# Kernel optimization log

Hardware: AMD Instinct MI355X
Metric: run time of the kernel (lower is better)

## Reference

```python
import jax, jax.numpy as jnp
import numpy as np

K_SELECT = 100      # select_box_nums_for_evaluation
IOU_THR = 0.7       # nms_iou_threshold
CONF_THR = 0.3      # confidence_score


def setup_inputs() -> dict:
    key = jax.random.key(0)
    k1, k2, k3 = jax.random.split(key, 3)
    B, Q, C = 256, 900, 91
    pred_logits = jax.random.normal(k1, (B, Q, C), dtype=jnp.float32)
    # cxcywh boxes in (0,1), strictly positive w/h
    pred_boxes = jax.random.uniform(k2, (B, Q, 4), dtype=jnp.float32, minval=0.05, maxval=0.45)
    # (img_h, img_w) per image
    target_sizes = jax.random.uniform(k3, (B, 2), dtype=jnp.float32, minval=200.0, maxval=1000.0)
    return {"pred_logits": pred_logits, "pred_boxes": pred_boxes, "target_sizes": target_sizes}


def _pairwise_iou(boxes):
    # boxes: [K,4] xyxy -> iou [K,K]
    area = (boxes[:, 2] - boxes[:, 0]) * (boxes[:, 3] - boxes[:, 1])
    lt = jnp.maximum(boxes[:, None, :2], boxes[None, :, :2])
    rb = jnp.minimum(boxes[:, None, 2:], boxes[None, :, 2:])
    wh = jnp.clip(rb - lt, 0.0)
    inter = wh[..., 0] * wh[..., 1]
    union = area[:, None] + area[None, :] - inter
    return inter / jnp.maximum(union, 1e-9)


def _nms_mask(boxes):
    # boxes already sorted by descending score (top_k output order).
    # Greedy NMS: box i suppresses lower-scored j if iou > IOU_THR and i itself kept.
    K = boxes.shape[0]
    iou = _pairwise_iou(boxes)
    rng = jnp.arange(K)

    def body(i, keep):
        suppress = (iou[i] > IOU_THR) & keep[i] & (rng > i)
        return keep & ~suppress

    return jax.lax.fori_loop(0, K, body, jnp.ones((K,), dtype=bool))


def reference(pred_logits, pred_boxes, target_sizes):
    B, Q, C = pred_logits.shape
    prob = jax.nn.sigmoid(pred_logits).reshape(B, Q * C)
    scores, topk_idx = jax.lax.top_k(prob, K_SELECT)        # [B,K] sorted desc
    topk_boxes = topk_idx // C                               # query index
    labels = topk_idx % C                                    # class index

    # cxcywh -> xyxy
    cxcy, wh = pred_boxes[..., :2], pred_boxes[..., 2:]
    xyxy = jnp.concatenate([cxcy - 0.5 * wh, cxcy + 0.5 * wh], axis=-1)  # [B,Q,4]
    boxes = jnp.take_along_axis(xyxy, topk_boxes[..., None], axis=1)     # [B,K,4]

    img_h, img_w = target_sizes[:, 0], target_sizes[:, 1]
    scale_fct = jnp.stack([img_w, img_h, img_w, img_h], axis=1)          # [B,4]
    boxes = boxes * scale_fct[:, None, :]

    conf_keep = scores > CONF_THR                            # confidence filter
    nms_keep = jax.vmap(_nms_mask)(boxes)                    # per-image NMS
    keep = conf_keep & nms_keep                              # fixed-shape mask (ragged lists in torch)
    return scores, labels, boxes, keep
```

## Files before the change

kernel.cpp:

```cpp
#include <hip/hip_runtime.h>
#include <stdint.h>

#define NBATCH 256
#define NQ 900
#define NC 91
#define NQC (NQ * NC)
#define KSEL 100
#define IOU_THRF 0.7f
#define CONF_THRF 0.3f
#define TH_LOGIT 2.2f
#define DELTA 4096u

#define SLC 8
#define SF4FULL 2560
#define SF4LAST 2555
#define ANT 256
#define SCAP 256
#define CAPB (SLC * SCAP)

#define BNT 512
#define HBINS 64
#define SRTCAP 512

__device__ __forceinline__ uint32_t fkey(float x) {
  uint32_t b = __float_as_uint(x);
  return b ^ ((uint32_t)((int32_t)b >> 31) | 0x80000000u);
}
__device__ __forceinline__ float unfkey(uint32_t k) {
  uint32_t b = (k & 0x80000000u) ? (k ^ 0x80000000u) : ~k;
  return __uint_as_float(b);
}
__device__ __forceinline__ float sigmoidf_ref(float x) {
  return 1.0f / (1.0f + expf(-x));
}

__global__ __launch_bounds__(ANT) void kfilter(const float* __restrict__ logits,
                                               uint32_t* __restrict__ cnts,
                                               unsigned long long* __restrict__ cand) {
  __shared__ unsigned long long lbuf[SCAP];
  __shared__ uint32_t lcnt;

  const int blk = blockIdx.x;
  const int b = blk / SLC;
  const int s = blk - b * SLC;
  const int tid = threadIdx.x;
  const int sf4 = (s == SLC - 1) ? SF4LAST : SF4FULL;
  const float4* lg4 = (const float4*)(logits + (size_t)b * NQC) + (size_t)s * SF4FULL;

  if (tid == 0) lcnt = 0;
  __syncthreads();

  for (int i = tid; i < sf4; i += ANT) {
    float4 v = lg4[i];
    const uint32_t ibase = (uint32_t)((s * SF4FULL + i) * 4);
    if (v.x >= TH_LOGIT) {
      uint32_t p = atomicAdd(&lcnt, 1u);
      if (p < SCAP) lbuf[p] = (((unsigned long long)fkey(v.x)) << 32) | (ibase + 0);
    }
    if (v.y >= TH_LOGIT) {
      uint32_t p = atomicAdd(&lcnt, 1u);
      if (p < SCAP) lbuf[p] = (((unsigned long long)fkey(v.y)) << 32) | (ibase + 1);
    }
    if (v.z >= TH_LOGIT) {
      uint32_t p = atomicAdd(&lcnt, 1u);
      if (p < SCAP) lbuf[p] = (((unsigned long long)fkey(v.z)) << 32) | (ibase + 2);
    }
    if (v.w >= TH_LOGIT) {
      uint32_t p = atomicAdd(&lcnt, 1u);
      if (p < SCAP) lbuf[p] = (((unsigned long long)fkey(v.w)) << 32) | (ibase + 3);
    }
  }
  __syncthreads();
  const uint32_t m = lcnt;
  if (tid == 0) cnts[blk] = m;
  const uint32_t mw = m < SCAP ? m : SCAP;
  for (uint32_t i = tid; i < mw; i += ANT)
    cand[(size_t)blk * SCAP + i] = lbuf[i];
}

union BSMem {
  struct {
    unsigned long long keys[CAPB];
    unsigned long long srt[SRTCAP];
    unsigned long long ranked[KSEL];
  } p;
  struct {
    float iou[KSEL * KSEL];
    float box[KSEL][4];
    int keep[KSEL];
  } nms;
};

__global__ __launch_bounds__(BNT) void merge_nms(const uint32_t* __restrict__ cnts,
                                                 const unsigned long long* __restrict__ cand,
                                                 const float* __restrict__ logits,
                                                 const float* __restrict__ pboxes,
                                                 const float* __restrict__ tsizes,
                                                 float* __restrict__ out,
                                                 int force_fallback) {
  __shared__ BSMem sm;
  __shared__ unsigned long long rankbuf[KSEL];
  __shared__ uint32_t scnt[SLC], soff[SLC];
  __shared__ uint32_t s_hist[HBINS];
  __shared__ uint32_t s_n, s_bad, s_cut, s_m;
  __shared__ unsigned long long red[BNT / 64];
  __shared__ unsigned long long s_last;

  const int b = blockIdx.x;
  const int tid = threadIdx.x;
  const float* lg = logits + (size_t)b * NQC;

  bool good = !force_fallback;
  if (good) {
    if (tid < SLC) scnt[tid] = cnts[b * SLC + tid];
    __syncthreads();
    if (tid == 0) {
      uint32_t off = 0, bad = 0;
      for (int i = 0; i < SLC; i++) {
        soff[i] = off;
        if (scnt[i] > SCAP) bad = 1;
        off += scnt[i];
      }
      s_n = off;
      s_bad = bad | (off < KSEL ? 1u : 0u);
    }
    __syncthreads();
    good = (s_bad == 0);
  }
  const uint32_t n = good ? s_n : 0;

  if (good) {
    const int wid = tid >> 6, lane = tid & 63;
    for (int sl = wid; sl < SLC; sl += BNT / 64) {
      const uint32_t c = scnt[sl], o = soff[sl];
      for (uint32_t j = lane; j < c; j += 64)
        sm.p.keys[o + j] = cand[((size_t)b * SLC + sl) * SCAP + j];
    }
    if (tid < HBINS) s_hist[tid] = 0;
    if (tid == 0) s_m = 0;
    __syncthreads();

    for (uint32_t i = tid; i < n; i += BNT) {
      uint32_t k = (uint32_t)(sm.p.keys[i] >> 32);
      uint32_t bin = (k >> 20) - 0xC00u;
      if (bin > HBINS - 1) bin = HBINS - 1;
      atomicAdd(&s_hist[bin], 1u);
    }
    __syncthreads();

    if (tid < 64) {
      uint32_t h = s_hist[tid];
      uint32_t suf = h;
      #pragma unroll
      for (int off = 1; off < 64; off <<= 1) {
        uint32_t t = __shfl_down(suf, off);
        if (tid + off < 64) suf += t;
      }
      bool pred = (suf >= KSEL) && (suf - h < KSEL);
      unsigned long long mask = __ballot(pred);
      int cutlane = __ffsll((long long)mask) - 1;
      if (tid == 0) s_cut = (uint32_t)cutlane;
    }
    __syncthreads();
    const uint32_t cut = s_cut;
    if (cut >= HBINS - 1) good = false;
    const uint32_t thresh = ((cut + 0xC00u) << 20) - DELTA;

    if (good) {
      for (uint32_t i = tid; i < n; i += BNT) {
        unsigned long long key = sm.p.keys[i];
        uint32_t k = (uint32_t)(key >> 32);
        if (k >= thresh) {
          uint32_t pb = __float_as_uint(sigmoidf_ref(unfkey(k)));
          uint32_t pos = atomicAdd(&s_m, 1u);
          if (pos < SRTCAP)
            sm.p.srt[pos] = (((unsigned long long)(~pb)) << 32) |
                            (key & 0xFFFFFFFFULL);
        }
      }
      __syncthreads();
      const uint32_t m = s_m;
      if (m > SRTCAP) good = false;
      if (good) {
        for (uint32_t q = tid; q < m; q += BNT) {
          unsigned long long mykey = sm.p.srt[q];
          uint32_t r = 0;
          for (uint32_t j = 0; j < m; j++)
            r += (sm.p.srt[j] < mykey) ? 1u : 0u;
          if (r < KSEL) rankbuf[r] = mykey;
        }
        __syncthreads();
      }
    }
  }

  if (!good) {
    unsigned long long last = ~0ULL;
    for (int r = 0; r < KSEL; r++) {
      unsigned long long best = 0ULL;
      for (int i = tid; i < NQC; i += BNT) {
        uint32_t pb = __float_as_uint(sigmoidf_ref(lg[i]));
        unsigned long long cmp = (((unsigned long long)pb) << 32) |
                                 (unsigned long long)(~(uint32_t)i);
        if (cmp < last && cmp > best) best = cmp;
      }
      #pragma unroll
      for (int o = 32; o >= 1; o >>= 1) {
        unsigned long long other = __shfl_down(best, o);
        if (other > best) best = other;
      }
      if ((tid & 63) == 0) red[tid >> 6] = best;
      __syncthreads();
      if (tid == 0) {
        unsigned long long mx = red[0];
        for (int w = 1; w < BNT / 64; w++) if (red[w] > mx) mx = red[w];
        s_last = mx;
        uint32_t pb = (uint32_t)(mx >> 32);
        uint32_t id = ~(uint32_t)mx;
        rankbuf[r] = (((unsigned long long)(~pb)) << 32) | (unsigned long long)id;
      }
      __syncthreads();
      last = s_last;
    }
  }

  float score = 0.0f;
  int idx = 0;
  if (tid < KSEL) {
    unsigned long long key = rankbuf[tid];
    score = __uint_as_float(~(uint32_t)(key >> 32));
    idx = (int)(uint32_t)(key & 0xFFFFFFFFu);
  }
  __syncthreads();

  const float img_h = tsizes[b * 2 + 0];
  const float img_w = tsizes[b * 2 + 1];
  float* out_scores = out;
  float* out_labels = out + (size_t)NBATCH * KSEL;
  float* out_boxes  = out + (size_t)2 * NBATCH * KSEL;
  float* out_keep   = out + (size_t)2 * NBATCH * KSEL + (size_t)NBATCH * KSEL * 4;

  if (tid < KSEL) {
    int q = idx / NC;
    int lab = idx - q * NC;
    const float* pb = pboxes + ((size_t)b * NQ + q) * 4;
    float cx = pb[0], cy = pb[1], w = pb[2], h = pb[3];
    float hw = __fmul_rn(0.5f, w), hh = __fmul_rn(0.5f, h);
    float x0 = __fmul_rn(__fsub_rn(cx, hw), img_w);
    float y0 = __fmul_rn(__fsub_rn(cy, hh), img_h);
    float x1 = __fmul_rn(__fadd_rn(cx, hw), img_w);
    float y1 = __fmul_rn(__fadd_rn(cy, hh), img_h);
    out_scores[(size_t)b * KSEL + tid] = score;
    out_labels[(size_t)b * KSEL + tid] = (float)lab;
    float* ob = out_boxes + ((size_t)b * KSEL + tid) * 4;
    ob[0] = x0; ob[1] = y0; ob[2] = x1; ob[3] = y1;
    sm.nms.box[tid][0] = x0; sm.nms.box[tid][1] = y0;
    sm.nms.box[tid][2] = x1; sm.nms.box[tid][3] = y1;
  }
  __syncthreads();

  for (int e = tid; e < KSEL * KSEL; e += BNT) {
    int i = e / KSEL;
    int j = e - i * KSEL;
    float ax0 = sm.nms.box[i][0], ay0 = sm.nms.box[i][1];
    float ax1 = sm.nms.box[i][2], ay1 = sm.nms.box[i][3];
    float bx0 = sm.nms.box[j][0], by0 = sm.nms.box[j][1];
    float bx1 = sm.nms.box[j][2], by1 = sm.nms.box[j][3];
    float areaA = __fmul_rn(__fsub_rn(ax1, ax0), __fsub_rn(ay1, ay0));
    float areaB = __fmul_rn(__fsub_rn(bx1, bx0), __fsub_rn(by1, by0));
    float ltx = fmaxf(ax0, bx0), lty = fmaxf(ay0, by0);
    float rbx = fminf(ax1, bx1), rby = fminf(ay1, by1);
    float wx = fmaxf(__fsub_rn(rbx, ltx), 0.0f);
    float wy = fmaxf(__fsub_rn(rby, lty), 0.0f);
    float inter = __fmul_rn(wx, wy);
    float uni = __fsub_rn(__fadd_rn(areaA, areaB), inter);
    sm.nms.iou[e] = __fdiv_rn(inter, fmaxf(uni, 1e-9f));
  }
  __syncthreads();

  if (tid < 64) {
    int keepA = 1;
    int keepB = 1;
    for (int i = 0; i < KSEL; i++) {
      int owner = i & 63;
      int ki = (i < 64) ? __shfl(keepA, owner) : __shfl(keepB, owner);
      if (ki) {
        if (tid > i && sm.nms.iou[i * KSEL + tid] > IOU_THRF) keepA = 0;
        int j = tid + 64;
        if (j < KSEL && j > i && sm.nms.iou[i * KSEL + j] > IOU_THRF) keepB = 0;
      }
    }
    sm.nms.keep[tid] = keepA;
    if (tid + 64 < KSEL) sm.nms.keep[tid + 64] = keepB;
  }
  __syncthreads();

  if (tid < KSEL) {
    float kp = (score > CONF_THRF && sm.nms.keep[tid]) ? 1.0f : 0.0f;
    out_keep[(size_t)b * KSEL + tid] = kp;
  }
}

extern "C" void kernel_launch(void* const* d_in, const int* in_sizes, int n_in,
                              void* d_out, int out_size, void* d_ws, size_t ws_size,
                              hipStream_t stream) {
  const float* logits = (const float*)d_in[0];
  const float* pboxes = (const float*)d_in[1];
  const float* tsizes = (const float*)d_in[2];
  (void)in_sizes; (void)n_in; (void)out_size;

  const size_t cnt_bytes = ((size_t)NBATCH * SLC * sizeof(uint32_t) + 255) & ~(size_t)255;
  const size_t need = cnt_bytes +
                      (size_t)NBATCH * SLC * SCAP * sizeof(unsigned long long);
  if (ws_size >= need) {
    uint32_t* cnts = (uint32_t*)d_ws;
    unsigned long long* cand = (unsigned long long*)((char*)d_ws + cnt_bytes);
    kfilter<<<NBATCH * SLC, ANT, 0, stream>>>(logits, cnts, cand);
    merge_nms<<<NBATCH, BNT, 0, stream>>>(cnts, cand, logits, pboxes, tsizes,
                                          (float*)d_out, 0);
  } else {
    merge_nms<<<NBATCH, BNT, 0, stream>>>(nullptr, nullptr, logits, pboxes, tsizes,
                                          (float*)d_out, 1);
  }
}
```

Baseline: 47.54 us.

## Fuse candidate filter into single per-image postprocessing kernel

Merges the separate filtering kernel (8 slices per image, 2048 blocks) into the merge/NMS kernel, so each 1024-thread block scans its image's logits directly and appends candidates into shared memory. This removes the second launch and the global workspace round trip for candidates and counts. In exchange, only 256 blocks stream the 84 MB logits tensor, which lowers memory-level parallelism on a GPU with many CUs, and a single shared-memory atomic counter per block becomes a contention point.

```diff
diff --git a/kernel.cpp b/kernel.cpp
--- a/kernel.cpp
+++ b/kernel.cpp
@@ -5,20 +5,15 @@
 #define NQ 900
 #define NC 91
 #define NQC (NQ * NC)
+#define NV4 (NQC / 4)
 #define KSEL 100
 #define IOU_THRF 0.7f
 #define CONF_THRF 0.3f
 #define TH_LOGIT 2.2f
 #define DELTA 4096u
 
-#define SLC 8
-#define SF4FULL 2560
-#define SF4LAST 2555
-#define ANT 256
-#define SCAP 256
-#define CAPB (SLC * SCAP)
-
-#define BNT 512
+#define NT 1024
+#define CAPB 2048
 #define HBINS 64
 #define SRTCAP 512
 
@@ -34,55 +29,10 @@
   return 1.0f / (1.0f + expf(-x));
 }
 
-__global__ __launch_bounds__(ANT) void kfilter(const float* __restrict__ logits,
-                                               uint32_t* __restrict__ cnts,
-                                               unsigned long long* __restrict__ cand) {
-  __shared__ unsigned long long lbuf[SCAP];
-  __shared__ uint32_t lcnt;
-
-  const int blk = blockIdx.x;
-  const int b = blk / SLC;
-  const int s = blk - b * SLC;
-  const int tid = threadIdx.x;
-  const int sf4 = (s == SLC - 1) ? SF4LAST : SF4FULL;
-  const float4* lg4 = (const float4*)(logits + (size_t)b * NQC) + (size_t)s * SF4FULL;
-
-  if (tid == 0) lcnt = 0;
-  __syncthreads();
-
-  for (int i = tid; i < sf4; i += ANT) {
-    float4 v = lg4[i];
-    const uint32_t ibase = (uint32_t)((s * SF4FULL + i) * 4);
-    if (v.x >= TH_LOGIT) {
-      uint32_t p = atomicAdd(&lcnt, 1u);
-      if (p < SCAP) lbuf[p] = (((unsigned long long)fkey(v.x)) << 32) | (ibase + 0);
-    }
-    if (v.y >= TH_LOGIT) {
-      uint32_t p = atomicAdd(&lcnt, 1u);
-      if (p < SCAP) lbuf[p] = (((unsigned long long)fkey(v.y)) << 32) | (ibase + 1);
-    }
-    if (v.z >= TH_LOGIT) {
-      uint32_t p = atomicAdd(&lcnt, 1u);
-      if (p < SCAP) lbuf[p] = (((unsigned long long)fkey(v.z)) << 32) | (ibase + 2);
-    }
-    if (v.w >= TH_LOGIT) {
-      uint32_t p = atomicAdd(&lcnt, 1u);
-      if (p < SCAP) lbuf[p] = (((unsigned long long)fkey(v.w)) << 32) | (ibase + 3);
-    }
-  }
-  __syncthreads();
-  const uint32_t m = lcnt;
-  if (tid == 0) cnts[blk] = m;
-  const uint32_t mw = m < SCAP ? m : SCAP;
-  for (uint32_t i = tid; i < mw; i += ANT)
-    cand[(size_t)blk * SCAP + i] = lbuf[i];
-}
-
-union BSMem {
+union SMem {
   struct {
     unsigned long long keys[CAPB];
     unsigned long long srt[SRTCAP];
-    unsigned long long ranked[KSEL];
   } p;
   struct {
     float iou[KSEL * KSEL];
@@ -91,56 +41,55 @@
   } nms;
 };
 
-__global__ __launch_bounds__(BNT) void merge_nms(const uint32_t* __restrict__ cnts,
-                                                 const unsigned long long* __restrict__ cand,
-                                                 const float* __restrict__ logits,
-                                                 const float* __restrict__ pboxes,
-                                                 const float* __restrict__ tsizes,
-                                                 float* __restrict__ out,
-                                                 int force_fallback) {
-  __shared__ BSMem sm;
+__global__ __launch_bounds__(NT) void postproc(const float* __restrict__ logits,
+                                               const float* __restrict__ pboxes,
+                                               const float* __restrict__ tsizes,
+                                               float* __restrict__ out) {
+  __shared__ SMem sm;
   __shared__ unsigned long long rankbuf[KSEL];
-  __shared__ uint32_t scnt[SLC], soff[SLC];
   __shared__ uint32_t s_hist[HBINS];
-  __shared__ uint32_t s_n, s_bad, s_cut, s_m;
-  __shared__ unsigned long long red[BNT / 64];
+  __shared__ uint32_t s_lcnt, s_cut, s_m;
+  __shared__ unsigned long long red[NT / 64];
   __shared__ unsigned long long s_last;
 
   const int b = blockIdx.x;
   const int tid = threadIdx.x;
   const float* lg = logits + (size_t)b * NQC;
-
-  bool good = !force_fallback;
+  const float4* lg4 = (const float4*)lg;
+
+  if (tid == 0) s_lcnt = 0;
+  __syncthreads();
+
+  for (int i = tid; i < NV4; i += NT) {
+    float4 v = lg4[i];
+    const uint32_t ibase = (uint32_t)(i * 4);
+    if (v.x >= TH_LOGIT) {
+      uint32_t p = atomicAdd(&s_lcnt, 1u);
+      if (p < CAPB) sm.p.keys[p] = (((unsigned long long)fkey(v.x)) << 32) | (ibase + 0);
+    }
+    if (v.y >= TH_LOGIT) {
+      uint32_t p = atomicAdd(&s_lcnt, 1u);
+      if (p < CAPB) sm.p.keys[p] = (((unsigned long long)fkey(v.y)) << 32) | (ibase + 1);
+    }
+    if (v.z >= TH_LOGIT) {
+      uint32_t p = atomicAdd(&s_lcnt, 1u);
+      if (p < CAPB) sm.p.keys[p] = (((unsigned long long)fkey(v.z)) << 32) | (ibase + 2);
+    }
+    if (v.w >= TH_LOGIT) {
+      uint32_t p = atomicAdd(&s_lcnt, 1u);
+      if (p < CAPB) sm.p.keys[p] = (((unsigned long long)fkey(v.w)) << 32) | (ibase + 3);
+    }
+  }
+  __syncthreads();
+  const uint32_t n = s_lcnt;
+  bool good = (n >= KSEL && n <= CAPB);
+
   if (good) {
-    if (tid < SLC) scnt[tid] = cnts[b * SLC + tid];
-    __syncthreads();
-    if (tid == 0) {
-      uint32_t off = 0, bad = 0;
-      for (int i = 0; i < SLC; i++) {
-        soff[i] = off;
-        if (scnt[i] > SCAP) bad = 1;
-        off += scnt[i];
-      }
-      s_n = off;
-      s_bad = bad | (off < KSEL ? 1u : 0u);
-    }
-    __syncthreads();
-    good = (s_bad == 0);
-  }
-  const uint32_t n = good ? s_n : 0;
-
-  if (good) {
-    const int wid = tid >> 6, lane = tid & 63;
-    for (int sl = wid; sl < SLC; sl += BNT / 64) {
-      const uint32_t c = scnt[sl], o = soff[sl];
-      for (uint32_t j = lane; j < c; j += 64)
-        sm.p.keys[o + j] = cand[((size_t)b * SLC + sl) * SCAP + j];
-    }
     if (tid < HBINS) s_hist[tid] = 0;
     if (tid == 0) s_m = 0;
     __syncthreads();
 
-    for (uint32_t i = tid; i < n; i += BNT) {
+    for (uint32_t i = tid; i < n; i += NT) {
       uint32_t k = (uint32_t)(sm.p.keys[i] >> 32);
       uint32_t bin = (k >> 20) - 0xC00u;
       if (bin > HBINS - 1) bin = HBINS - 1;
@@ -167,7 +116,7 @@
     const uint32_t thresh = ((cut + 0xC00u) << 20) - DELTA;
 
     if (good) {
-      for (uint32_t i = tid; i < n; i += BNT) {
+      for (uint32_t i = tid; i < n; i += NT) {
         unsigned long long key = sm.p.keys[i];
         uint32_t k = (uint32_t)(key >> 32);
         if (k >= thresh) {
@@ -182,7 +131,7 @@
       const uint32_t m = s_m;
       if (m > SRTCAP) good = false;
       if (good) {
-        for (uint32_t q = tid; q < m; q += BNT) {
+        for (uint32_t q = tid; q < m; q += NT) {
           unsigned long long mykey = sm.p.srt[q];
           uint32_t r = 0;
           for (uint32_t j = 0; j < m; j++)
@@ -198,7 +147,7 @@
     unsigned long long last = ~0ULL;
     for (int r = 0; r < KSEL; r++) {
       unsigned long long best = 0ULL;
-      for (int i = tid; i < NQC; i += BNT) {
+      for (int i = tid; i < NQC; i += NT) {
         uint32_t pb = __float_as_uint(sigmoidf_ref(lg[i]));
         unsigned long long cmp = (((unsigned long long)pb) << 32) |
                                  (unsigned long long)(~(uint32_t)i);
@@ -213,7 +162,7 @@
       __syncthreads();
       if (tid == 0) {
         unsigned long long mx = red[0];
-        for (int w = 1; w < BNT / 64; w++) if (red[w] > mx) mx = red[w];
+        for (int w = 1; w < NT / 64; w++) if (red[w] > mx) mx = red[w];
         s_last = mx;
         uint32_t pb = (uint32_t)(mx >> 32);
         uint32_t id = ~(uint32_t)mx;
@@ -259,7 +208,7 @@
   }
   __syncthreads();
 
-  for (int e = tid; e < KSEL * KSEL; e += BNT) {
+  for (int e = tid; e < KSEL * KSEL; e += NT) {
     int i = e / KSEL;
     int j = e - i * KSEL;
     float ax0 = sm.nms.box[i][0], ay0 = sm.nms.box[i][1];
@@ -307,19 +256,6 @@
   const float* logits = (const float*)d_in[0];
   const float* pboxes = (const float*)d_in[1];
   const float* tsizes = (const float*)d_in[2];
-  (void)in_sizes; (void)n_in; (void)out_size;
-
-  const size_t cnt_bytes = ((size_t)NBATCH * SLC * sizeof(uint32_t) + 255) & ~(size_t)255;
-  const size_t need = cnt_bytes +
-                      (size_t)NBATCH * SLC * SCAP * sizeof(unsigned long long);
-  if (ws_size >= need) {
-    uint32_t* cnts = (uint32_t*)d_ws;
-    unsigned long long* cand = (unsigned long long*)((char*)d_ws + cnt_bytes);
-    kfilter<<<NBATCH * SLC, ANT, 0, stream>>>(logits, cnts, cand);
-    merge_nms<<<NBATCH, BNT, 0, stream>>>(cnts, cand, logits, pboxes, tsizes,
-                                          (float*)d_out, 0);
-  } else {
-    merge_nms<<<NBATCH, BNT, 0, stream>>>(nullptr, nullptr, logits, pboxes, tsizes,
-                                          (float*)d_out, 1);
-  }
-}
+  (void)in_sizes; (void)n_in; (void)out_size; (void)d_ws; (void)ws_size;
+  postproc<<<NBATCH, NT, 0, stream>>>(logits, pboxes, tsizes, (float*)d_out);
+}
```

Measured after the change: 45.50 us. -4.3%, faster.
